# Kernel tuning notes

Measured on AMD Instinct MI355X. Metric: run time of the kernel, lower is better.

## Reference

```python
import jax, jax.numpy as jnp
from jax import lax
import numpy as np

D_MODEL = 1024
D_STATE = 16
D_CONV = 4
EXPAND = 2
D_INNER = EXPAND * D_MODEL
BATCH = 2
SEQLEN = 1024


def setup_inputs() -> dict:
    key = jax.random.key(0)
    ks = jax.random.split(key, 8)
    x = jax.random.normal(ks[0], (BATCH, SEQLEN, D_MODEL), jnp.float32)
    W_in = jax.random.normal(ks[1], (2 * D_INNER, D_MODEL), jnp.float32) * (1.0 / np.sqrt(D_MODEL))
    conv_w = jax.random.normal(ks[2], (D_INNER, 1, D_CONV), jnp.float32) * (1.0 / np.sqrt(D_CONV))
    conv_b = jax.random.normal(ks[3], (D_INNER,), jnp.float32) * 0.02
    W_x = jax.random.normal(ks[4], (2 * D_STATE, D_INNER), jnp.float32) * (1.0 / np.sqrt(D_INNER))
    W_dt = jax.random.normal(ks[5], (D_INNER, D_INNER), jnp.float32) * (1.0 / np.sqrt(D_INNER))
    b_dt = jax.random.normal(ks[6], (D_INNER,), jnp.float32) * 0.02
    # A_log = log(arange(1..d_state)) repeated over d_inner rows, as in __init__
    A_log = jnp.log(jnp.tile(jnp.arange(1, D_STATE + 1, dtype=jnp.float32), (D_INNER, 1)))
    D = jnp.ones((D_INNER,), jnp.float32)
    W_out = jax.random.normal(ks[7], (D_MODEL, D_INNER), jnp.float32) * (1.0 / np.sqrt(D_INNER))
    return {"x": x, "W_in": W_in, "conv_w": conv_w, "conv_b": conv_b,
            "W_x": W_x, "W_dt": W_dt, "b_dt": b_dt, "A_log": A_log,
            "D": D, "W_out": W_out}


def reference(x, W_in, conv_w, conv_b, W_x, W_dt, b_dt, A_log, D, W_out):
    d_inner, _, d_conv = conv_w.shape
    d_state = A_log.shape[1]

    # in_proj and split into x / gate z
    xz = x @ W_in.T                                   # (B, L, 2*d_inner)
    xi, z = jnp.split(xz, 2, axis=-1)

    # causal depthwise conv1d: torch pads both sides by d_conv-1 then slices
    # [:seqlen], which equals left-only padding of d_conv-1
    xc = lax.conv_general_dilated(
        xi.transpose(0, 2, 1), conv_w, window_strides=(1,),
        padding=[(d_conv - 1, 0)],
        dimension_numbers=("NCH", "OIH", "NCH"),
        feature_group_count=d_inner)
    xc = xc + conv_b[None, :, None]
    u = jax.nn.silu(xc.transpose(0, 2, 1))            # (B, L, d_inner)

    # input-dependent B, C and dt
    BC = u @ W_x.T                                    # (B, L, 2*d_state)
    Bmat, Cmat = jnp.split(BC, 2, axis=-1)
    dt = jax.nn.softplus(u @ W_dt.T + b_dt)           # (B, L, d_inner)

    A = -jnp.exp(A_log)                               # (d_inner, d_state)
    dA = jnp.exp(dt[..., None] * A)                   # (B, L, d_inner, d_state)
    dBu = dt[..., None] * Bmat[:, :, None, :] * u[..., None]

    def step(s, inp):
        dA_t, dBu_t, C_t = inp
        s = dA_t * s + dBu_t                          # (B, d_inner, d_state)
        y_t = jnp.einsum("bdn,bn->bd", s, C_t)
        return s, y_t

    s0 = jnp.zeros((x.shape[0], d_inner, d_state), x.dtype)
    _, ys = lax.scan(step, s0,
                     (dA.transpose(1, 0, 2, 3),
                      dBu.transpose(1, 0, 2, 3),
                      Cmat.transpose(1, 0, 2)))
    y = ys.transpose(1, 0, 2) + D * u                 # (B, L, d_inner)

    y = y * jax.nn.silu(z)
    # dropout is identity in eval mode
    return y @ W_out.T
```

## Files before the change

### kernel.cpp

```cpp
#include <hip/hip_runtime.h>
#include <hip/hip_bf16.h>
#include <math.h>

#define B_SZ   2
#define LSEQ   1024
#define DMODEL 1024
#define DSTATE 16
#define DCONV  4
#define DINNER 2048
#define MROWS  (B_SZ * LSEQ)
#define NCHUNK 32
#define TCHUNK (LSEQ / NCHUNK)
#define NCAT   2176
#define BKS    64

typedef __attribute__((ext_vector_type(8))) short bf16x8;
typedef __attribute__((ext_vector_type(4))) float f32x4;

__device__ __forceinline__ void gl2lds16(const void* g, void* l) {
    __builtin_amdgcn_global_load_lds(
        (const __attribute__((address_space(1))) void*)g,
        (__attribute__((address_space(3))) void*)l, 16, 0, 0);
}

__global__ __launch_bounds__(256)
void cvt_bf16(const float* __restrict__ in, __hip_bfloat16* __restrict__ out)
{
    int i = (blockIdx.x * 256 + threadIdx.x) * 8;
    float4 a = *(const float4*)&in[i];
    float4 b = *(const float4*)&in[i + 4];
    union { __hip_bfloat16 h[8]; int4 v; } o;
    o.h[0] = __float2bfloat16(a.x); o.h[1] = __float2bfloat16(a.y);
    o.h[2] = __float2bfloat16(a.z); o.h[3] = __float2bfloat16(a.w);
    o.h[4] = __float2bfloat16(b.x); o.h[5] = __float2bfloat16(b.y);
    o.h[6] = __float2bfloat16(b.z); o.h[7] = __float2bfloat16(b.w);
    *(int4*)&out[i] = o.v;
}

template<int EPI>
__global__ __launch_bounds__(256)
void gemm_bt(const __hip_bfloat16* __restrict__ A,
             const __hip_bfloat16* __restrict__ B,
             const float* __restrict__ bias,
             float* __restrict__ Cbase, size_t pstride, int ldc,
             float* __restrict__ C2,
             int K, int klen)
{
    constexpr int BN   = 64;
    constexpr int NLD  = (128 + BN) / 8 / 4;
    constexpr int SMEL = (128 + BN) * BKS;
    __shared__ __hip_bfloat16 sm[2 * SMEL];

    const int tid  = threadIdx.x;
    const int lane = tid & 63;
    const int w    = tid >> 6;
    const int m0 = blockIdx.x * 128;
    const int n0 = blockIdx.y * BN;
    const int wr = w >> 1, wc = w & 1;
    const int kbase = blockIdx.z * klen;
    float* __restrict__ C = Cbase + (size_t)blockIdx.z * pstride;

    const int lrow = lane >> 3;
    const int swc  = ((lane & 7) ^ lrow) * 8;
    const __hip_bfloat16* srcp[NLD];
    #pragma unroll
    for (int i = 0; i < NLD; ++i) {
        const int q = w + 4 * i;
        srcp[i] = (q < 16)
            ? A + (size_t)(m0 + q * 8 + lrow) * K + kbase + swc
            : B + (size_t)(n0 + (q - 16) * 8 + lrow) * K + kbase + swc;
    }

    f32x4 acc[4][2] = {};
    const int l7 = lane & 7, l15 = lane & 15, lq = lane >> 4;
    const int sw0 = (lq ^ l7) * 8;
    const int sw1 = sw0 ^ 32;

    #pragma unroll
    for (int i = 0; i < NLD; ++i)
        gl2lds16(srcp[i], sm + (w + 4 * i) * 512);
    asm volatile("s_waitcnt vmcnt(0)" ::: "memory");
    __builtin_amdgcn_s_barrier();
    __builtin_amdgcn_sched_barrier(0);

    const int nt = klen / BKS;
    int buf = 0;
    for (int t = 0; t < nt; ++t) {
        if (t + 1 < nt) {
            #pragma unroll
            for (int i = 0; i < NLD; ++i)
                gl2lds16(srcp[i] + (size_t)(t + 1) * BKS,
                         sm + (buf ^ 1) * SMEL + (w + 4 * i) * 512);
        }
        const __hip_bfloat16* As = sm + buf * SMEL;
        const __hip_bfloat16* Bs = As + 128 * BKS;
        bf16x8 a0[4], a1[4], b0[2], b1[2];
        #pragma unroll
        for (int m = 0; m < 4; ++m) {
            const int r = (wr * 64 + m * 16 + l15) * BKS;
            a0[m] = *(const bf16x8*)&As[r + sw0];
            a1[m] = *(const bf16x8*)&As[r + sw1];
        }
        #pragma unroll
        for (int n = 0; n < 2; ++n) {
            const int r = (wc * 32 + n * 16 + l15) * BKS;
            b0[n] = *(const bf16x8*)&Bs[r + sw0];
            b1[n] = *(const bf16x8*)&Bs[r + sw1];
        }
        #pragma unroll
        for (int m = 0; m < 4; ++m)
            #pragma unroll
            for (int n = 0; n < 2; ++n) {
                acc[m][n] = __builtin_amdgcn_mfma_f32_16x16x32_bf16(
                    a0[m], b0[n], acc[m][n], 0, 0, 0);
                acc[m][n] = __builtin_amdgcn_mfma_f32_16x16x32_bf16(
                    a1[m], b1[n], acc[m][n], 0, 0, 0);
            }
        asm volatile("s_waitcnt vmcnt(0)" ::: "memory");
        __builtin_amdgcn_s_barrier();
        __builtin_amdgcn_sched_barrier(0);
        buf ^= 1;
    }

    #pragma unroll
    for (int m = 0; m < 4; ++m)
        #pragma unroll
        for (int n = 0; n < 2; ++n) {
            const int col = n0 + wc * 32 + n * 16 + l15;
            #pragma unroll
            for (int j = 0; j < 4; ++j) {
                const int row = m0 + wr * 64 + m * 16 + lq * 4 + j;
                float v = acc[m][n][j];
                if (EPI == 0) {
                    C[(size_t)row * ldc + col] = v;
                } else {
                    if (col < DINNER) {
                        v += bias[col];
                        v = (v > 20.f) ? v : log1pf(__expf(v));
                        C[(size_t)row * ldc + col] = v;
                    } else if (col < DINNER + 32) {
                        C2[(size_t)row * 32 + (col - DINNER)] = v;
                    }
                }
            }
        }
}

__global__ __launch_bounds__(256)
void add4(const float* __restrict__ p, float* __restrict__ o)
{
    const size_t S = (size_t)MROWS * DMODEL;
    int i = (blockIdx.x * 256 + threadIdx.x) * 4;
    float4 a = *(const float4*)&p[i];
    float4 b = *(const float4*)&p[i + S];
    float4 c = *(const float4*)&p[i + 2 * S];
    float4 d = *(const float4*)&p[i + 3 * S];
    a.x += b.x + c.x + d.x; a.y += b.y + c.y + d.y;
    a.z += b.z + c.z + d.z; a.w += b.w + c.w + d.w;
    *(float4*)&o[i] = a;
}

__global__ __launch_bounds__(256)
void conv_silu(const float* __restrict__ xz, const float* __restrict__ cw,
               const float* __restrict__ cb, float* __restrict__ u,
               __hip_bfloat16* __restrict__ u_bf)
{
    int idx = blockIdx.x * blockDim.x + threadIdx.x;
    int d = idx & (DINNER - 1);
    int m = idx >> 11;
    int t = m & (LSEQ - 1);
    float acc = cb[d];
    #pragma unroll
    for (int j = 0; j < DCONV; ++j) {
        int tt = t - (DCONV - 1) + j;
        if (tt >= 0)
            acc += xz[(size_t)(m - t + tt) * 4096 + d] * cw[d * DCONV + j];
    }
    float v = acc / (1.f + __expf(-acc));
    u[(size_t)m * DINNER + d] = v;
    u_bf[(size_t)m * DINNER + d] = __float2bfloat16(v);
}

__global__ __launch_bounds__(256)
void scan_part1(const float* __restrict__ dt, const float* __restrict__ u,
                const float* __restrict__ bc, const float* __restrict__ A_log,
                float* __restrict__ s_end, float* __restrict__ dtsum)
{
    const int d = blockIdx.x * 256 + threadIdx.x;
    const int c = blockIdx.y;
    const int b = blockIdx.z;
    __shared__ float bcs[TCHUNK][32];
    {
        int f = threadIdx.x * 4;
        const float* src = bc + ((size_t)b * LSEQ + c * TCHUNK) * 32;
        *(float4*)&bcs[f >> 5][f & 31] = *(const float4*)&src[f];
    }
    float An[16];
    {
        float4 a0 = *(const float4*)&A_log[d * DSTATE + 0];
        float4 a1 = *(const float4*)&A_log[d * DSTATE + 4];
        float4 a2 = *(const float4*)&A_log[d * DSTATE + 8];
        float4 a3 = *(const float4*)&A_log[d * DSTATE + 12];
        An[0]=-__expf(a0.x); An[1]=-__expf(a0.y); An[2]=-__expf(a0.z); An[3]=-__expf(a0.w);
        An[4]=-__expf(a1.x); An[5]=-__expf(a1.y); An[6]=-__expf(a1.z); An[7]=-__expf(a1.w);
        An[8]=-__expf(a2.x); An[9]=-__expf(a2.y); An[10]=-__expf(a2.z); An[11]=-__expf(a2.w);
        An[12]=-__expf(a3.x); An[13]=-__expf(a3.y); An[14]=-__expf(a3.z); An[15]=-__expf(a3.w);
    }
    __syncthreads();
    const float* dtp = dt + ((size_t)b * LSEQ + c * TCHUNK) * DINNER + d;
    const float* up  = u  + ((size_t)b * LSEQ + c * TCHUNK) * DINNER + d;
    float s[16] = {};
    float sum = 0.f;
    for (int t = 0; t < TCHUNK; ++t) {
        float dtv = dtp[(size_t)t * DINNER];
        float uv  = up [(size_t)t * DINNER];
        sum += dtv;
        float du = dtv * uv;
        #pragma unroll
        for (int n = 0; n < 16; ++n) {
            float a = __expf(dtv * An[n]);
            s[n] = a * s[n] + du * bcs[t][n];
        }
    }
    float* se = s_end + ((size_t)(b * NCHUNK + c) * DINNER + d) * 16;
    #pragma unroll
    for (int q = 0; q < 4; ++q)
        *(float4*)&se[q * 4] = make_float4(s[q*4], s[q*4+1], s[q*4+2], s[q*4+3]);
    dtsum[(size_t)(b * NCHUNK + c) * DINNER + d] = sum;
}

__global__ __launch_bounds__(256)
void scan_combine(float* __restrict__ s_end, const float* __restrict__ dtsum,
                  const float* __restrict__ A_log)
{
    int idx = blockIdx.x * 256 + threadIdx.x;
    int n = idx & 15;
    int d = (idx >> 4) & (DINNER - 1);
    int b = idx >> 15;
    float An = -__expf(A_log[d * DSTATE + n]);
    float s = 0.f;
    for (int c = 0; c < NCHUNK; ++c) {
        size_t base = (size_t)(b * NCHUNK + c) * DINNER + d;
        float se = s_end[base * 16 + n];
        s_end[base * 16 + n] = s;
        float P = __expf(An * dtsum[base]);
        s = P * s + se;
    }
}

__global__ __launch_bounds__(256)
void scan_part2(const float* __restrict__ dt, const float* __restrict__ u,
                const float* __restrict__ bc, const float* __restrict__ s_in,
                const float* __restrict__ A_log, const float* __restrict__ Dp,
                const float* __restrict__ xz, __hip_bfloat16* __restrict__ y_bf)
{
    const int d = blockIdx.x * 256 + threadIdx.x;
    const int c = blockIdx.y;
    const int b = blockIdx.z;
    __shared__ float bcs[TCHUNK][32];
    {
        int f = threadIdx.x * 4;
        const float* src = bc + ((size_t)b * LSEQ + c * TCHUNK) * 32;
        *(float4*)&bcs[f >> 5][f & 31] = *(const float4*)&src[f];
    }
    float An[16];
    {
        float4 a0 = *(const float4*)&A_log[d * DSTATE + 0];
        float4 a1 = *(const float4*)&A_log[d * DSTATE + 4];
        float4 a2 = *(const float4*)&A_log[d * DSTATE + 8];
        float4 a3 = *(const float4*)&A_log[d * DSTATE + 12];
        An[0]=-__expf(a0.x); An[1]=-__expf(a0.y); An[2]=-__expf(a0.z); An[3]=-__expf(a0.w);
        An[4]=-__expf(a1.x); An[5]=-__expf(a1.y); An[6]=-__expf(a1.z); An[7]=-__expf(a1.w);
        An[8]=-__expf(a2.x); An[9]=-__expf(a2.y); An[10]=-__expf(a2.z); An[11]=-__expf(a2.w);
        An[12]=-__expf(a3.x); An[13]=-__expf(a3.y); An[14]=-__expf(a3.z); An[15]=-__expf(a3.w);
    }
    float s[16];
    {
        const float* si = s_in + ((size_t)(b * NCHUNK + c) * DINNER + d) * 16;
        #pragma unroll
        for (int q = 0; q < 4; ++q) {
            float4 v = *(const float4*)&si[q * 4];
            s[q*4] = v.x; s[q*4+1] = v.y; s[q*4+2] = v.z; s[q*4+3] = v.w;
        }
    }
    const float Dd = Dp[d];
    __syncthreads();
    const float* dtp = dt + ((size_t)b * LSEQ + c * TCHUNK) * DINNER + d;
    const float* up  = u  + ((size_t)b * LSEQ + c * TCHUNK) * DINNER + d;
    const float* zp  = xz + ((size_t)b * LSEQ + c * TCHUNK) * 4096 + 2048 + d;
    __hip_bfloat16* yp = y_bf + ((size_t)b * LSEQ + c * TCHUNK) * DINNER + d;
    for (int t = 0; t < TCHUNK; ++t) {
        float dtv = dtp[(size_t)t * DINNER];
        float uv  = up [(size_t)t * DINNER];
        float du = dtv * uv;
        float y = Dd * uv;
        #pragma unroll
        for (int n = 0; n < 16; ++n) {
            float a = __expf(dtv * An[n]);
            s[n] = a * s[n] + du * bcs[t][n];
            y += s[n] * bcs[t][16 + n];
        }
        float zv = zp[(size_t)t * 4096];
        yp[(size_t)t * DINNER] = __float2bfloat16(y * (zv / (1.f + __expf(-zv))));
    }
}

extern "C" void kernel_launch(void* const* d_in, const int* in_sizes, int n_in,
                              void* d_out, int out_size, void* d_ws, size_t ws_size,
                              hipStream_t stream)
{
    const float* x      = (const float*)d_in[0];
    const float* W_in   = (const float*)d_in[1];
    const float* conv_w = (const float*)d_in[2];
    const float* conv_b = (const float*)d_in[3];
    const float* W_x    = (const float*)d_in[4];
    const float* W_dt   = (const float*)d_in[5];
    const float* b_dt   = (const float*)d_in[6];
    const float* A_log  = (const float*)d_in[7];
    const float* Dp     = (const float*)d_in[8];
    const float* W_out  = (const float*)d_in[9];
    float* out = (float*)d_out;

    const size_t MB = 1ull << 20;
    char* w8 = (char*)d_ws;
    float* xz    = (float*)(w8);
    float* p3    = (float*)(w8);
    float* u     = (float*)(w8 + 32*MB);
    float* dtc   = (float*)(w8 + 48*MB);
    float* bc    = (float*)(w8 + 64*MB);
    float* sbuf  = (float*)(w8 + 65*MB);
    float* dtsum = (float*)(w8 + 73*MB);
    __hip_bfloat16* u_bf   = (__hip_bfloat16*)(w8 + 74*MB);
    __hip_bfloat16* x_bf   = (__hip_bfloat16*)(w8 + 82*MB);
    __hip_bfloat16* Win_bf = (__hip_bfloat16*)(w8 + 86*MB);
    __hip_bfloat16* Wcat_bf= (__hip_bfloat16*)(w8 + 82*MB);
    __hip_bfloat16* Wout_bf= (__hip_bfloat16*)(w8 + 90*MB + 512*1024);
    __hip_bfloat16* y_bf   = (__hip_bfloat16*)(w8 + 82*MB);
    Wout_bf = (__hip_bfloat16*)(w8 + 90*MB);

    cvt_bf16<<<(MROWS * DMODEL) / 2048, 256, 0, stream>>>(x, x_bf);
    cvt_bf16<<<(4096 * DMODEL) / 2048, 256, 0, stream>>>(W_in, Win_bf);
    gemm_bt<0><<<dim3(16, 64, 1), 256, 0, stream>>>(
        x_bf, Win_bf, nullptr, xz, 0, 4096, nullptr, DMODEL, DMODEL);
    conv_silu<<<(MROWS * DINNER) / 256, 256, 0, stream>>>(xz, conv_w, conv_b, u, u_bf);
    cvt_bf16<<<(DINNER * DINNER) / 2048, 256, 0, stream>>>(W_dt, Wcat_bf);
    cvt_bf16<<<(32 * DINNER) / 2048, 256, 0, stream>>>(W_x, Wcat_bf + (size_t)DINNER * DINNER);
    gemm_bt<2><<<dim3(16, NCAT / 64, 1), 256, 0, stream>>>(
        u_bf, Wcat_bf, b_dt, dtc, 0, DINNER, bc, DINNER, DINNER);
    cvt_bf16<<<(DMODEL * DINNER) / 2048, 256, 0, stream>>>(W_out, Wout_bf);
    scan_part1<<<dim3(DINNER/256, NCHUNK, B_SZ), 256, 0, stream>>>(
        dtc, u, bc, A_log, sbuf, dtsum);
    scan_combine<<<(B_SZ * DINNER * DSTATE) / 256, 256, 0, stream>>>(
        sbuf, dtsum, A_log);
    scan_part2<<<dim3(DINNER/256, NCHUNK, B_SZ), 256, 0, stream>>>(
        dtc, u, bc, sbuf, A_log, Dp, xz, y_bf);
    gemm_bt<0><<<dim3(16, 16, 4), 256, 0, stream>>>(
        y_bf, Wout_bf, nullptr, p3, (size_t)MROWS * DMODEL, DMODEL, nullptr,
        DINNER, DINNER / 4);
    add4<<<(MROWS * DMODEL) / 1024, 256, 0, stream>>>(p3, out);
}
```

Before: 194.4 us.

## Merge bf16 conversions, drop fp32 u buffer, halve out-proj split-K

All five fp32-to-bf16 conversion launches are merged into one kernel that picks its source by block index. The fp32 copy of u is no longer written, and both scan kernels read the bf16 u instead, which cuts memory traffic but lowers precision in the D*u term and in dBu. The output projection's split-K drops from 4 to 2, so the final reduction reads two partials instead of four, at the cost of fewer GEMM blocks for parallelism.

After: 184.0 us. -5.3%, faster.

```diff
diff --git a/kernel.cpp b/kernel.cpp
--- a/kernel.cpp
+++ b/kernel.cpp
@@ -23,10 +23,9 @@
         (__attribute__((address_space(3))) void*)l, 16, 0, 0);
 }
 
-__global__ __launch_bounds__(256)
-void cvt_bf16(const float* __restrict__ in, __hip_bfloat16* __restrict__ out)
-{
-    int i = (blockIdx.x * 256 + threadIdx.x) * 8;
+__device__ __forceinline__ void cvt8(const float* __restrict__ in,
+                                     __hip_bfloat16* __restrict__ out, int i)
+{
     float4 a = *(const float4*)&in[i];
     float4 b = *(const float4*)&in[i + 4];
     union { __hip_bfloat16 h[8]; int4 v; } o;
@@ -35,6 +34,23 @@
     o.h[4] = __float2bfloat16(b.x); o.h[5] = __float2bfloat16(b.y);
     o.h[6] = __float2bfloat16(b.z); o.h[7] = __float2bfloat16(b.w);
     *(int4*)&out[i] = o.v;
+}
+
+__global__ __launch_bounds__(256)
+void cvt_all(const float* __restrict__ x,    __hip_bfloat16* __restrict__ xb,
+             const float* __restrict__ win,  __hip_bfloat16* __restrict__ winb,
+             const float* __restrict__ wdt,  const float* __restrict__ wx,
+             __hip_bfloat16* __restrict__ wcat,
+             const float* __restrict__ wout, __hip_bfloat16* __restrict__ woutb)
+{
+    const int b = blockIdx.x;
+    const int t8 = threadIdx.x * 8;
+    if      (b < 1024) cvt8(x,    xb,    b * 2048 + t8);
+    else if (b < 3072) cvt8(win,  winb,  (b - 1024) * 2048 + t8);
+    else if (b < 5120) cvt8(wdt,  wcat,  (b - 3072) * 2048 + t8);
+    else if (b < 5152) cvt8(wx,   wcat + (size_t)DINNER * DINNER,
+                                         (b - 5120) * 2048 + t8);
+    else               cvt8(wout, woutb, (b - 5152) * 2048 + t8);
 }
 
 template<int EPI>
@@ -147,23 +163,19 @@
 }
 
 __global__ __launch_bounds__(256)
-void add4(const float* __restrict__ p, float* __restrict__ o)
-{
-    const size_t S = (size_t)MROWS * DMODEL;
+void add2(const float* __restrict__ a, const float* __restrict__ b,
+          float* __restrict__ o)
+{
     int i = (blockIdx.x * 256 + threadIdx.x) * 4;
-    float4 a = *(const float4*)&p[i];
-    float4 b = *(const float4*)&p[i + S];
-    float4 c = *(const float4*)&p[i + 2 * S];
-    float4 d = *(const float4*)&p[i + 3 * S];
-    a.x += b.x + c.x + d.x; a.y += b.y + c.y + d.y;
-    a.z += b.z + c.z + d.z; a.w += b.w + c.w + d.w;
-    *(float4*)&o[i] = a;
+    float4 va = *(const float4*)&a[i];
+    float4 vb = *(const float4*)&b[i];
+    va.x += vb.x; va.y += vb.y; va.z += vb.z; va.w += vb.w;
+    *(float4*)&o[i] = va;
 }
 
 __global__ __launch_bounds__(256)
 void conv_silu(const float* __restrict__ xz, const float* __restrict__ cw,
-               const float* __restrict__ cb, float* __restrict__ u,
-               __hip_bfloat16* __restrict__ u_bf)
+               const float* __restrict__ cb, __hip_bfloat16* __restrict__ u_bf)
 {
     int idx = blockIdx.x * blockDim.x + threadIdx.x;
     int d = idx & (DINNER - 1);
@@ -177,12 +189,11 @@
             acc += xz[(size_t)(m - t + tt) * 4096 + d] * cw[d * DCONV + j];
     }
     float v = acc / (1.f + __expf(-acc));
-    u[(size_t)m * DINNER + d] = v;
     u_bf[(size_t)m * DINNER + d] = __float2bfloat16(v);
 }
 
 __global__ __launch_bounds__(256)
-void scan_part1(const float* __restrict__ dt, const float* __restrict__ u,
+void scan_part1(const float* __restrict__ dt, const __hip_bfloat16* __restrict__ u,
                 const float* __restrict__ bc, const float* __restrict__ A_log,
                 float* __restrict__ s_end, float* __restrict__ dtsum)
 {
@@ -208,12 +219,12 @@
     }
     __syncthreads();
     const float* dtp = dt + ((size_t)b * LSEQ + c * TCHUNK) * DINNER + d;
-    const float* up  = u  + ((size_t)b * LSEQ + c * TCHUNK) * DINNER + d;
+    const __hip_bfloat16* up = u + ((size_t)b * LSEQ + c * TCHUNK) * DINNER + d;
     float s[16] = {};
     float sum = 0.f;
     for (int t = 0; t < TCHUNK; ++t) {
         float dtv = dtp[(size_t)t * DINNER];
-        float uv  = up [(size_t)t * DINNER];
+        float uv  = __bfloat162float(up[(size_t)t * DINNER]);
         sum += dtv;
         float du = dtv * uv;
         #pragma unroll
@@ -249,7 +260,7 @@
 }
 
 __global__ __launch_bounds__(256)
-void scan_part2(const float* __restrict__ dt, const float* __restrict__ u,
+void scan_part2(const float* __restrict__ dt, const __hip_bfloat16* __restrict__ u,
                 const float* __restrict__ bc, const float* __restrict__ s_in,
                 const float* __restrict__ A_log, const float* __restrict__ Dp,
                 const float* __restrict__ xz, __hip_bfloat16* __restrict__ y_bf)
@@ -286,12 +297,12 @@
     const float Dd = Dp[d];
     __syncthreads();
     const float* dtp = dt + ((size_t)b * LSEQ + c * TCHUNK) * DINNER + d;
-    const float* up  = u  + ((size_t)b * LSEQ + c * TCHUNK) * DINNER + d;
+    const __hip_bfloat16* up = u + ((size_t)b * LSEQ + c * TCHUNK) * DINNER + d;
     const float* zp  = xz + ((size_t)b * LSEQ + c * TCHUNK) * 4096 + 2048 + d;
     __hip_bfloat16* yp = y_bf + ((size_t)b * LSEQ + c * TCHUNK) * DINNER + d;
     for (int t = 0; t < TCHUNK; ++t) {
         float dtv = dtp[(size_t)t * DINNER];
-        float uv  = up [(size_t)t * DINNER];
+        float uv  = __bfloat162float(up[(size_t)t * DINNER]);
         float du = dtv * uv;
         float y = Dd * uv;
         #pragma unroll
@@ -325,37 +336,33 @@
     char* w8 = (char*)d_ws;
     float* xz    = (float*)(w8);
     float* p3    = (float*)(w8);
-    float* u     = (float*)(w8 + 32*MB);
-    float* dtc   = (float*)(w8 + 48*MB);
-    float* bc    = (float*)(w8 + 64*MB);
-    float* sbuf  = (float*)(w8 + 65*MB);
-    float* dtsum = (float*)(w8 + 73*MB);
-    __hip_bfloat16* u_bf   = (__hip_bfloat16*)(w8 + 74*MB);
-    __hip_bfloat16* x_bf   = (__hip_bfloat16*)(w8 + 82*MB);
-    __hip_bfloat16* Win_bf = (__hip_bfloat16*)(w8 + 86*MB);
-    __hip_bfloat16* Wcat_bf= (__hip_bfloat16*)(w8 + 82*MB);
-    __hip_bfloat16* Wout_bf= (__hip_bfloat16*)(w8 + 90*MB + 512*1024);
-    __hip_bfloat16* y_bf   = (__hip_bfloat16*)(w8 + 82*MB);
-    Wout_bf = (__hip_bfloat16*)(w8 + 90*MB);
-
-    cvt_bf16<<<(MROWS * DMODEL) / 2048, 256, 0, stream>>>(x, x_bf);
-    cvt_bf16<<<(4096 * DMODEL) / 2048, 256, 0, stream>>>(W_in, Win_bf);
+    __hip_bfloat16* u_bf = (__hip_bfloat16*)(w8 + 32*MB);
+    float* dtc   = (float*)(w8 + 40*MB);
+    float* bc    = (float*)(w8 + 56*MB);
+    float* sbuf  = (float*)(w8 + 57*MB);
+    float* dtsum = (float*)(w8 + 65*MB);
+    __hip_bfloat16* x_bf   = (__hip_bfloat16*)(w8 + 66*MB);
+    __hip_bfloat16* Win_bf = (__hip_bfloat16*)(w8 + 70*MB);
+    __hip_bfloat16* y_bf   = (__hip_bfloat16*)(w8 + 66*MB);
+    __hip_bfloat16* Wcat_bf= (__hip_bfloat16*)(w8 + 78*MB);
+    __hip_bfloat16* Wout_bf= (__hip_bfloat16*)(w8 + 86*MB + 512*1024);
+
+    cvt_all<<<6176, 256, 0, stream>>>(x, x_bf, W_in, Win_bf,
+                                      W_dt, W_x, Wcat_bf, W_out, Wout_bf);
     gemm_bt<0><<<dim3(16, 64, 1), 256, 0, stream>>>(
         x_bf, Win_bf, nullptr, xz, 0, 4096, nullptr, DMODEL, DMODEL);
-    conv_silu<<<(MROWS * DINNER) / 256, 256, 0, stream>>>(xz, conv_w, conv_b, u, u_bf);
-    cvt_bf16<<<(DINNER * DINNER) / 2048, 256, 0, stream>>>(W_dt, Wcat_bf);
-    cvt_bf16<<<(32 * DINNER) / 2048, 256, 0, stream>>>(W_x, Wcat_bf + (size_t)DINNER * DINNER);
+    conv_silu<<<(MROWS * DINNER) / 256, 256, 0, stream>>>(xz, conv_w, conv_b, u_bf);
     gemm_bt<2><<<dim3(16, NCAT / 64, 1), 256, 0, stream>>>(
         u_bf, Wcat_bf, b_dt, dtc, 0, DINNER, bc, DINNER, DINNER);
-    cvt_bf16<<<(DMODEL * DINNER) / 2048, 256, 0, stream>>>(W_out, Wout_bf);
     scan_part1<<<dim3(DINNER/256, NCHUNK, B_SZ), 256, 0, stream>>>(
-        dtc, u, bc, A_log, sbuf, dtsum);
+        dtc, u_bf, bc, A_log, sbuf, dtsum);
     scan_combine<<<(B_SZ * DINNER * DSTATE) / 256, 256, 0, stream>>>(
         sbuf, dtsum, A_log);
     scan_part2<<<dim3(DINNER/256, NCHUNK, B_SZ), 256, 0, stream>>>(
-        dtc, u, bc, sbuf, A_log, Dp, xz, y_bf);
-    gemm_bt<0><<<dim3(16, 16, 4), 256, 0, stream>>>(
+        dtc, u_bf, bc, sbuf, A_log, Dp, xz, y_bf);
+    gemm_bt<0><<<dim3(16, 16, 2), 256, 0, stream>>>(
         y_bf, Wout_bf, nullptr, p3, (size_t)MROWS * DMODEL, DMODEL, nullptr,
-        DINNER, DINNER / 4);
-    add4<<<(MROWS * DMODEL) / 1024, 256, 0, stream>>>(p3, out);
-}
+        DINNER, DINNER / 2);
+    add2<<<(MROWS * DMODEL) / 1024, 256, 0, stream>>>(
+        p3, p3 + (size_t)MROWS * DMODEL, out);
+}
```
